# Optimization experiments

Measured on AMD Instinct MI355X. Metric: run time of the kernel, lower is better.

## Reference

```python
import jax, jax.numpy as jnp
import numpy as np

IN_FEAT = 66; D_MODEL = 512; KS = 10; DCT_N = 20; NUM_STAGE = 2; BN_EPS = 1e-5
HID = D_MODEL; GCN_IN = 2 * DCT_N


def get_dct_matrix(N):
    k = np.arange(N)[:, None]; i = np.arange(N)[None, :]
    w = np.full((N, 1), np.sqrt(2.0 / N)); w[0, 0] = np.sqrt(1.0 / N)
    dct = (w * np.cos(np.pi * (i + 0.5) * k / N)).astype(np.float32)
    idct = np.linalg.inv(dct).astype(np.float32)
    return jnp.asarray(dct), jnp.asarray(idct)


def conv1d(x, w):
    # x: [B, Cin, L], w: [Cout, Cin, K] -> [B, Cout, L-K+1]
    return jax.lax.conv_general_dilated(x, w, (1,), 'VALID', dimension_numbers=('NCH', 'OIH', 'NCH'))


def _forward(src, Wq1, Wq2, Wk1, Wk2, gc1_W, gc1_att, gc1_b, bn1_g, bn1_b,
             gcb_W, gcb_att, gcb_b, gcb_bn_g, gcb_bn_b, gc7_W, gc7_att, gc7_b,
             output_n, input_n):
    bs = src.shape[0]
    src = src[:, :input_n]                                  # [B, 50, F]
    vl = KS + output_n                                      # 35
    vn = input_n - KS - output_n + 1                        # 16
    dct_m, idct_m = get_dct_matrix(vl)

    key_in = jnp.swapaxes(src, 1, 2)[:, :, :input_n - output_n] / 1000.0   # [B, F, 25]
    query_in = jnp.swapaxes(src, 1, 2)[:, :, -KS:] / 1000.0                # [B, F, 10]

    # overlapping sliding windows -> per-window DCT coefficients
    idx = np.arange(vl)[None, :] + np.arange(vn)[:, None]   # [vn, vl]
    val = src[:, idx]                                       # [B, vn, vl, F]
    val = jnp.einsum('kv,bnvf->bnfk', dct_m[:DCT_N], val).reshape(bs, vn, IN_FEAT * DCT_N)

    key = jax.nn.relu(conv1d(jax.nn.relu(conv1d(key_in, Wk1)), Wk2))       # [B, D, vn]
    query = jax.nn.relu(conv1d(jax.nn.relu(conv1d(query_in, Wq1)), Wq2))   # [B, D, 1]

    score = jnp.einsum('bdq,bdn->bqn', query, key) + 1e-15                 # [B, 1, vn]
    att = score / jnp.sum(score, axis=2, keepdims=True)                    # sum-normalized attention
    dct_att = jnp.einsum('bqn,bnf->bqf', att, val)[:, 0].reshape(bs, IN_FEAT, DCT_N)

    # last KS frames + last frame repeated output_n times
    idx2 = np.concatenate([np.arange(input_n - KS, input_n), np.full(output_n, input_n - 1)])
    input_gcn = src[:, idx2]                                               # [B, vl, F]
    dct_in = jnp.swapaxes(jnp.einsum('kv,bvf->bkf', dct_m[:DCT_N], input_gcn), 1, 2)  # [B, F, DCT_N]
    x = jnp.concatenate([dct_in, dct_att], axis=-1)                        # [B, F, 2*DCT_N]

    # ---- GCN (eval mode: dropout off, BN with fresh running stats mean=0, var=1) ----
    def gc(y, W, A, bias):
        return jnp.einsum('nm,bmf->bnf', A, y @ W) + bias

    def bn(y, g, be):
        b_, n_, f_ = y.shape
        v = y.reshape(b_, n_ * f_)
        v = v * (g / np.float32(np.sqrt(1.0 + BN_EPS))) + be
        return v.reshape(b_, n_, f_)

    y = jnp.tanh(bn(gc(x, gc1_W, gc1_att, gc1_b), bn1_g, bn1_b))
    for st in range(NUM_STAGE):
        y0 = y
        y = jnp.tanh(bn(gc(y, gcb_W[st, 0], gcb_att[st, 0], gcb_b[st, 0]), gcb_bn_g[st, 0], gcb_bn_b[st, 0]))
        y = jnp.tanh(bn(gc(y, gcb_W[st, 1], gcb_att[st, 1], gcb_b[st, 1]), gcb_bn_g[st, 1], gcb_bn_b[st, 1]))
        y = y + y0
    dct_out = gc(y, gc7_W, gc7_att, gc7_b) + x                             # [B, F, 2*DCT_N]

    out = jnp.einsum('vk,bfk->bvf', idct_m[:, :DCT_N], dct_out[:, :, :DCT_N])  # [B, vl, F]
    return out[:, :, None, :]                                              # [B, vl, itera=1, F]


def setup_inputs():
    key = jax.random.key(0)
    ks = jax.random.split(key, 11)
    bs = 512; s = 0.05; f32 = jnp.float32
    return {
        'src': jax.random.normal(ks[0], (bs, 50, IN_FEAT), f32),
        'Wq1': jax.random.normal(ks[1], (D_MODEL, IN_FEAT, 6), f32) * s,
        'Wq2': jax.random.normal(ks[2], (D_MODEL, D_MODEL, 5), f32) * s,
        'Wk1': jax.random.normal(ks[3], (D_MODEL, IN_FEAT, 6), f32) * s,
        'Wk2': jax.random.normal(ks[4], (D_MODEL, D_MODEL, 5), f32) * s,
        'gc1_W': jax.random.normal(ks[5], (GCN_IN, HID), f32) * s,
        'gc1_att': jax.random.normal(ks[6], (IN_FEAT, IN_FEAT), f32) * s,
        'gc1_b': jnp.zeros((HID,), f32),
        'bn1_g': jnp.ones((IN_FEAT * HID,), f32),
        'bn1_b': jnp.zeros((IN_FEAT * HID,), f32),
        'gcb_W': jax.random.normal(ks[7], (NUM_STAGE, 2, HID, HID), f32) * s,
        'gcb_att': jax.random.normal(ks[8], (NUM_STAGE, 2, IN_FEAT, IN_FEAT), f32) * s,
        'gcb_b': jnp.zeros((NUM_STAGE, 2, HID), f32),
        'gcb_bn_g': jnp.ones((NUM_STAGE, 2, IN_FEAT * HID), f32),
        'gcb_bn_b': jnp.zeros((NUM_STAGE, 2, IN_FEAT * HID), f32),
        'gc7_W': jax.random.normal(ks[9], (HID, GCN_IN), f32) * s,
        'gc7_att': jax.random.normal(ks[10], (IN_FEAT, IN_FEAT), f32) * s,
        'gc7_b': jnp.zeros((GCN_IN,), f32),
        'output_n': 25,
        'input_n': 50,
    }


def reference(src, Wq1, Wq2, Wk1, Wk2, gc1_W, gc1_att, gc1_b, bn1_g, bn1_b,
              gcb_W, gcb_att, gcb_b, gcb_bn_g, gcb_bn_b, gc7_W, gc7_att, gc7_b,
              output_n, input_n):
    return _forward(src, Wq1, Wq2, Wk1, Wk2, gc1_W, gc1_att, gc1_b, bn1_g, bn1_b,
                    gcb_W, gcb_att, gcb_b, gcb_bn_g, gcb_bn_b, gc7_W, gc7_att, gc7_b,
                    output_n, input_n)
```

## Files before the change

### kernel.cpp

```cpp
#include <hip/hip_runtime.h>
#include <math.h>

#define PI_D 3.14159265358979323846

#define BSZ   512
#define NODE  66
#define VL    35
#define DCTN  20

static constexpr float BN_INVS = 0.99999500003749969f;

typedef unsigned short u16;
using bf16x8 = __attribute__((ext_vector_type(8))) short;
using f32x4  = __attribute__((ext_vector_type(4))) float;

__device__ inline u16 f2bf(float f) {
    union { float f; unsigned int u; } v; v.f = f;
    unsigned int r = v.u + 0x7FFFu + ((v.u >> 16) & 1u);
    return (u16)(r >> 16);
}
__device__ inline float bf2f(u16 b) {
    union { unsigned int u; float f; } v; v.u = ((unsigned int)b) << 16;
    return v.f;
}

__global__ void dct_kernel(float* __restrict__ dct20) {
    int i = blockIdx.x * blockDim.x + threadIdx.x;
    if (i < DCTN * VL) {
        int k = i / VL, v = i - k * VL;
        double w = (k == 0) ? sqrt(1.0 / VL) : sqrt(2.0 / VL);
        dct20[i] = (float)(w * cos(PI_D * (v + 0.5) * k / (double)VL));
    }
}

__global__ void cvt_gcb(const float* __restrict__ W, u16* __restrict__ Wt) {
    int l = blockIdx.y;
    int i = blockIdx.x * 256 + threadIdx.x;
    int n = i >> 9, k = i & 511;
    Wt[(size_t)l * 262144 + i] = f2bf(W[(size_t)l * 262144 + (size_t)k * 512 + n]);
}
__global__ void cvt_gc1(const float* __restrict__ W, u16* __restrict__ Wt) {
    int i = blockIdx.x * 256 + threadIdx.x;
    int n = i >> 6, k = i & 63;
    Wt[i] = (k < 40) ? f2bf(W[k * 512 + n]) : (u16)0;
}
__global__ void cvt_gc7(const float* __restrict__ W, u16* __restrict__ Wt) {
    int i = blockIdx.x * 256 + threadIdx.x;
    int n = i >> 9, k = i & 511;
    Wt[i] = (n < 20) ? f2bf(W[k * 40 + n]) : (u16)0;
}
__global__ void cvt_w1(const float* __restrict__ W, u16* __restrict__ Wt) {
    int i = blockIdx.x * 256 + threadIdx.x;
    int d = i / 416, k = i - d * 416;
    float v = 0.f;
    if (k < 396) { int h = k / 66, c = k - h * 66; v = W[d * 396 + c * 6 + h]; }
    Wt[i] = f2bf(v);
}
__global__ void cvt_w2(const float* __restrict__ W, u16* __restrict__ Wt) {
    int i = blockIdx.x * 256 + threadIdx.x;
    int d = i / 2560, k = i - d * 2560;
    int h = k >> 9, c = k & 511;
    Wt[i] = f2bf(W[(size_t)d * 2560 + c * 5 + h]);
}
__global__ void cvt_att(const float* __restrict__ gc1A, const float* __restrict__ gcbA,
                        const float* __restrict__ gc7A, u16* __restrict__ Abf) {
    int l = blockIdx.y;
    int i = blockIdx.x * 256 + threadIdx.x;
    if (i < 8320) {
        int r = i / 104, c = i - (i / 104) * 104;
        float v = 0.f;
        if (r < 66 && c < 66) {
            const float* A = (l == 0) ? gc1A : (l <= 4 ? gcbA + (size_t)(l - 1) * 4356 : gc7A);
            v = A[r * 66 + c];
        }
        Abf[(size_t)l * 8320 + i] = f2bf(v);
    }
}

template<int FB, int NW>
__global__ __launch_bounds__(256) void amul(const u16* __restrict__ Y,
                                            const u16* __restrict__ Abf,
                                            u16* __restrict__ U) {
    const int b = blockIdx.x, f0 = blockIdx.y * FB;
    const int tid = threadIdx.x;
    __shared__ u16 As[80][104];
    __shared__ u16 Ys[FB][104];
    for (int i = tid; i < 4160; i += 256) ((unsigned int*)As)[i] = ((const unsigned int*)Abf)[i];
    for (int i = tid; i < 66 * (FB / 2); i += 256) {
        int m = i / (FB / 2), fi = i - (i / (FB / 2)) * (FB / 2);
        unsigned int v = *(const unsigned int*)&Y[((size_t)b * 66 + m) * NW + f0 + 2 * fi];
        Ys[2 * fi][m] = (u16)(v & 0xffff);
        Ys[2 * fi + 1][m] = (u16)(v >> 16);
    }
    for (int i = tid; i < FB * 19; i += 256) {
        int f = i / 19, j = i - (i / 19) * 19;
        ((unsigned int*)&Ys[f][66])[j] = 0;
    }
    __syncthreads();
    const int lane = tid & 63, w = tid >> 6;
    const int row16 = lane & 15, grp = lane >> 4;
    const int fbase = w * (FB / 4);
    constexpr int NFT = FB / 64;
    f32x4 acc[5][NFT] = {};
#pragma unroll
    for (int k0 = 0; k0 < 96; k0 += 32) {
        bf16x8 aF[5], bF[NFT];
#pragma unroll
        for (int mt = 0; mt < 5; ++mt) aF[mt] = *(const bf16x8*)&As[mt * 16 + row16][grp * 8 + k0];
#pragma unroll
        for (int ft = 0; ft < NFT; ++ft) bF[ft] = *(const bf16x8*)&Ys[fbase + ft * 16 + row16][grp * 8 + k0];
#pragma unroll
        for (int mt = 0; mt < 5; ++mt)
#pragma unroll
            for (int ft = 0; ft < NFT; ++ft)
                acc[mt][ft] = __builtin_amdgcn_mfma_f32_16x16x32_bf16(aF[mt], bF[ft], acc[mt][ft], 0, 0, 0);
    }
#pragma unroll
    for (int mt = 0; mt < 5; ++mt) {
#pragma unroll
        for (int ft = 0; ft < NFT; ++ft) {
            int fcol = f0 + fbase + ft * 16 + row16;
#pragma unroll
            for (int j = 0; j < 4; ++j) {
                int row = mt * 16 + grp * 4 + j;
                if (row < 66)
                    U[((size_t)b * 66 + row) * NW + fcol] = f2bf(acc[mt][ft][j]);
            }
        }
    }
}

template<int ASRC, int EPI, int TOUT, int TIN, int T0>
__global__ __launch_bounds__(256) void gemm_uni(const void* __restrict__ Asrc,
                                                const u16* __restrict__ Bt,
                                                void* __restrict__ Cout,
                                                int M, int K, int Nvalid, int ldc,
                                                const float* __restrict__ bias,
                                                const float* __restrict__ g,
                                                const float* __restrict__ be,
                                                const u16* __restrict__ yres,
                                                const float* __restrict__ xres) {
    __shared__ u16 As[128][40];
    __shared__ u16 Bs[128][40];
    const int tid = threadIdx.x;
    const int r0 = blockIdx.x * 128, n0 = blockIdx.y * 128;
    const int lane = tid & 63, w = tid >> 6;
    const int wr = (w >> 1) * 64, wc = (w & 1) * 64;
    const int row16 = lane & 15, grp = lane >> 4;
    const int sr = tid >> 1, sq = (tid & 1) * 16;

    const u16* ap = nullptr;
    const float* apf = nullptr;
    if constexpr (ASRC == 0) {
        ap = (const u16*)Asrc + (size_t)(r0 + sr) * K + sq;
    } else if constexpr (ASRC == 1) {
        int R = r0 + sr; int b = R / TOUT, t = R - b * TOUT;
        ap = (const u16*)Asrc + ((size_t)b * TIN + t) * 512 + sq;
    } else {
        int R = r0 + sr; int b = R / TOUT, t = R - b * TOUT;
        apf = (const float*)Asrc + (size_t)b * 3300 + (T0 + t) * 66 + sq;
    }
    const u16* bp = Bt + (size_t)(n0 + sr) * K + sq;

    f32x4 acc[4][4] = {};
    for (int k0 = 0; k0 < K; k0 += 32) {
        if constexpr (ASRC <= 1) {
            *(bf16x8*)&As[sr][sq]     = *(const bf16x8*)(ap + k0);
            *(bf16x8*)&As[sr][sq + 8] = *(const bf16x8*)(ap + k0 + 8);
        } else {
#pragma unroll
            for (int j = 0; j < 16; ++j) {
                int k = k0 + sq + j;
                float vin = 0.f;
                if (k < 396) vin = apf[k0 + j];
                As[sr][sq + j] = f2bf(vin * 1e-3f);
            }
        }
        *(bf16x8*)&Bs[sr][sq]     = *(const bf16x8*)(bp + k0);
        *(bf16x8*)&Bs[sr][sq + 8] = *(const bf16x8*)(bp + k0 + 8);
        __syncthreads();
        bf16x8 a[4], b[4];
#pragma unroll
        for (int m = 0; m < 4; ++m) a[m] = *(const bf16x8*)&As[wr + m * 16 + row16][grp * 8];
#pragma unroll
        for (int n = 0; n < 4; ++n) b[n] = *(const bf16x8*)&Bs[wc + n * 16 + row16][grp * 8];
#pragma unroll
        for (int m = 0; m < 4; ++m)
#pragma unroll
            for (int n = 0; n < 4; ++n)
                acc[m][n] = __builtin_amdgcn_mfma_f32_16x16x32_bf16(a[m], b[n], acc[m][n], 0, 0, 0);
        __syncthreads();
    }
#pragma unroll
    for (int m = 0; m < 4; ++m) {
        int rb = r0 + wr + m * 16 + grp * 4;
#pragma unroll
        for (int n = 0; n < 4; ++n) {
            int c = n0 + wc + n * 16 + row16;
            if (c < Nvalid) {
#pragma unroll
                for (int j = 0; j < 4; ++j) {
                    int row = rb + j;
                    float v = acc[m][n][j];
                    if constexpr (EPI == 0) {
                        ((u16*)Cout)[(size_t)row * ldc + c] = f2bf(fmaxf(v, 0.f));
                    } else if constexpr (EPI == 1) {
                        ((float*)Cout)[(size_t)row * ldc + c] = fmaxf(v, 0.f);
                    } else if constexpr (EPI == 2 || EPI == 3) {
                        int bb = row / 66, nn = row - bb * 66;
                        int gi = nn * 512 + c;
                        float z = v + bias[c];
                        float t = tanhf(z * (g[gi] * BN_INVS) + be[gi]);
                        if constexpr (EPI == 3) t += bf2f(yres[(size_t)row * 512 + c]);
                        ((u16*)Cout)[(size_t)row * 512 + c] = f2bf(t);
                    } else {
                        int bb = row / 66, nn = row - bb * 66;
                        ((float*)Cout)[(size_t)bb * 1320 + nn * 20 + c] =
                            v + bias[c] + xres[(size_t)bb * 2640 + nn * 40 + c];
                    }
                }
            }
        }
    }
}

__global__ __launch_bounds__(256) void att_kernel(const float* __restrict__ qT,
                                                  const float* __restrict__ kT,
                                                  float* __restrict__ att) {
    const int b = blockIdx.x, tid = threadIdx.x;
    __shared__ float part[256];
    __shared__ float sc[16];
    int n = tid >> 4, j = tid & 15;
    const float* q = qT + b * 512;
    const float* k = kT + b * 8192 + n * 512;
    float acc = 0.f;
    for (int d = j; d < 512; d += 16) acc += q[d] * k[d];
    part[tid] = acc;
    __syncthreads();
    if (tid < 16) {
        float s = 0.f;
        for (int jj = 0; jj < 16; ++jj) s += part[tid * 16 + jj];
        sc[tid] = s + 1e-15f;
    }
    __syncthreads();
    if (tid == 0) {
        float tot = 0.f;
        for (int nn = 0; nn < 16; ++nn) tot += sc[nn];
        float inv = 1.f / tot;
        for (int nn = 0; nn < 16; ++nn) att[b * 16 + nn] = sc[nn] * inv;
    }
}

__global__ __launch_bounds__(256) void xbuild(const float* __restrict__ src,
                                              const float* __restrict__ att,
                                              const float* __restrict__ dct20,
                                              float* __restrict__ x,
                                              u16* __restrict__ xbf) {
    const int b = blockIdx.x, tid = threadIdx.x;
    __shared__ float s_src[50 * 66];
    __shared__ float s_sacc[VL * 66];
    __shared__ float s_d[DCTN * VL];
    __shared__ float s_att[16];
    for (int i = tid; i < 3300; i += 256) s_src[i] = src[b * 3300 + i];
    for (int i = tid; i < DCTN * VL; i += 256) s_d[i] = dct20[i];
    if (tid < 16) s_att[tid] = att[b * 16 + tid];
    __syncthreads();
    for (int i = tid; i < VL * 66; i += 256) {
        int v = i / 66, f = i - (i / 66) * 66;
        float a = 0.f;
#pragma unroll
        for (int n = 0; n < 16; ++n) a += s_att[n] * s_src[(n + v) * 66 + f];
        s_sacc[i] = a;
    }
    __syncthreads();
    for (int i = tid; i < 66 * DCTN; i += 256) {
        int f = i / DCTN, kq = i - (i / DCTN) * DCTN;
        float din = 0.f, datt = 0.f;
        for (int v = 0; v < VL; ++v) {
            float dv = s_d[kq * VL + v];
            int t2 = (v < 10) ? (40 + v) : 49;
            din += dv * s_src[t2 * 66 + f];
            datt += dv * s_sacc[v * 66 + f];
        }
        x[b * 2640 + f * 40 + kq] = din;
        x[b * 2640 + f * 40 + 20 + kq] = datt;
        xbf[(size_t)b * 4224 + f * 64 + kq] = f2bf(din);
        xbf[(size_t)b * 4224 + f * 64 + 20 + kq] = f2bf(datt);
    }
    for (int i = tid; i < 66 * 24; i += 256) {
        int f = i / 24, kp = 40 + (i - (i / 24) * 24);
        xbf[(size_t)b * 4224 + f * 64 + kp] = 0;
    }
}

__global__ __launch_bounds__(256) void final_out(const float* __restrict__ dctout,
                                                 const float* __restrict__ dct20,
                                                 float* __restrict__ out) {
    const int b = blockIdx.x, tid = threadIdx.x;
    __shared__ float ds[DCTN * VL];
    __shared__ float dos[66 * 20];
    for (int i = tid; i < DCTN * VL; i += 256) ds[i] = dct20[i];
    for (int i = tid; i < 1320; i += 256) dos[i] = dctout[(size_t)b * 1320 + i];
    __syncthreads();
    for (int o = tid; o < VL * 66; o += 256) {
        int v = o / 66, f = o - (o / 66) * 66;
        float acc = 0.f;
#pragma unroll
        for (int k = 0; k < DCTN; ++k) acc += ds[k * VL + v] * dos[f * 20 + k];
        out[(size_t)b * 2310 + o] = acc;
    }
}

extern "C" void kernel_launch(void* const* d_in, const int* in_sizes, int n_in,
                              void* d_out, int out_size, void* d_ws, size_t ws_size,
                              hipStream_t stream) {
    const float* src     = (const float*)d_in[0];
    const float* Wq1     = (const float*)d_in[1];
    const float* Wq2     = (const float*)d_in[2];
    const float* Wk1     = (const float*)d_in[3];
    const float* Wk2     = (const float*)d_in[4];
    const float* gc1_W   = (const float*)d_in[5];
    const float* gc1_att = (const float*)d_in[6];
    const float* gc1_b   = (const float*)d_in[7];
    const float* bn1_g   = (const float*)d_in[8];
    const float* bn1_b   = (const float*)d_in[9];
    const float* gcb_W   = (const float*)d_in[10];
    const float* gcb_att = (const float*)d_in[11];
    const float* gcb_b   = (const float*)d_in[12];
    const float* gcb_g   = (const float*)d_in[13];
    const float* gcb_be  = (const float*)d_in[14];
    const float* gc7_W   = (const float*)d_in[15];
    const float* gc7_att = (const float*)d_in[16];
    const float* gc7_b   = (const float*)d_in[17];
    float* out = (float*)d_out;

    unsigned char* base = (unsigned char*)d_ws;
    size_t off = 0;
    auto take = [&](size_t bytes) -> void* {
        void* p = base + off;
        off += (bytes + 255) & ~(size_t)255;
        return p;
    };
    u16*   yA     = (u16*)take((size_t)33792 * 512 * 2);
    u16*   yB     = (u16*)take((size_t)33792 * 512 * 2);
    u16*   ub     = (u16*)take((size_t)33792 * 512 * 2);
    u16*   u1     = (u16*)take((size_t)33792 * 64 * 2);
    float* xb     = (float*)take((size_t)512 * 2640 * 4);
    u16*   xbf    = (u16*)take((size_t)512 * 4224 * 2);
    float* dct20  = (float*)take(2800);
    float* dctout = (float*)take((size_t)512 * 1320 * 4);
    u16*   key1   = (u16*)take((size_t)512 * 20 * 512 * 2);
    u16*   q1     = (u16*)take((size_t)512 * 5 * 512 * 2);
    float* keyT   = (float*)take((size_t)8192 * 512 * 4);
    float* queryT = (float*)take((size_t)512 * 512 * 4);
    float* attw   = (float*)take((size_t)512 * 16 * 4);
    u16*   WtGcb  = (u16*)take((size_t)4 * 512 * 512 * 2);
    u16*   WtGc1  = (u16*)take((size_t)512 * 64 * 2);
    u16*   WtGc7  = (u16*)take((size_t)128 * 512 * 2);
    u16*   WtW1k  = (u16*)take((size_t)512 * 416 * 2);
    u16*   WtW1q  = (u16*)take((size_t)512 * 416 * 2);
    u16*   WtW2k  = (u16*)take((size_t)512 * 2560 * 2);
    u16*   WtW2q  = (u16*)take((size_t)512 * 2560 * 2);
    u16*   Abf    = (u16*)take((size_t)6 * 8320 * 2);

    dct_kernel<<<2, 384, 0, stream>>>(dct20);
    cvt_att<<<dim3(33, 6), 256, 0, stream>>>(gc1_att, gcb_att, gc7_att, Abf);
    cvt_gcb<<<dim3(1024, 4), 256, 0, stream>>>(gcb_W, WtGcb);
    cvt_gc1<<<128, 256, 0, stream>>>(gc1_W, WtGc1);
    cvt_gc7<<<256, 256, 0, stream>>>(gc7_W, WtGc7);
    cvt_w1<<<832, 256, 0, stream>>>(Wk1, WtW1k);
    cvt_w1<<<832, 256, 0, stream>>>(Wq1, WtW1q);
    cvt_w2<<<5120, 256, 0, stream>>>(Wk2, WtW2k);
    cvt_w2<<<5120, 256, 0, stream>>>(Wq2, WtW2q);

    gemm_uni<2, 0, 20, 25, 0><<<dim3(80, 4), 256, 0, stream>>>(
        src, WtW1k, key1, 10240, 416, 512, 512, nullptr, nullptr, nullptr, nullptr, nullptr);
    gemm_uni<2, 0, 5, 10, 40><<<dim3(20, 4), 256, 0, stream>>>(
        src, WtW1q, q1, 2560, 416, 512, 512, nullptr, nullptr, nullptr, nullptr, nullptr);
    gemm_uni<1, 1, 16, 20, 0><<<dim3(64, 4), 256, 0, stream>>>(
        key1, WtW2k, keyT, 8192, 2560, 512, 512, nullptr, nullptr, nullptr, nullptr, nullptr);
    gemm_uni<1, 1, 1, 5, 0><<<dim3(4, 4), 256, 0, stream>>>(
        q1, WtW2q, queryT, 512, 2560, 512, 512, nullptr, nullptr, nullptr, nullptr, nullptr);
    att_kernel<<<BSZ, 256, 0, stream>>>(queryT, keyT, attw);
    xbuild<<<BSZ, 256, 0, stream>>>(src, attw, dct20, xb, xbf);

    amul<64, 64><<<dim3(512, 1), 256, 0, stream>>>(xbf, Abf, u1);
    gemm_uni<0, 2, 1, 1, 0><<<dim3(264, 4), 256, 0, stream>>>(
        u1, WtGc1, yA, 33792, 64, 512, 512, gc1_b, bn1_g, bn1_b, nullptr, nullptr);

    for (int st = 0; st < 2; ++st) {
        const u16* W0 = WtGcb + (size_t)(st * 2 + 0) * 262144;
        const u16* W1 = WtGcb + (size_t)(st * 2 + 1) * 262144;
        const u16* A0 = Abf + (size_t)(1 + st * 2) * 8320;
        const u16* A1 = Abf + (size_t)(2 + st * 2) * 8320;
        const float* b0  = gcb_b + (size_t)(st * 2 + 0) * 512;
        const float* b1  = gcb_b + (size_t)(st * 2 + 1) * 512;
        const float* g0  = gcb_g + (size_t)(st * 2 + 0) * 33792;
        const float* g1  = gcb_g + (size_t)(st * 2 + 1) * 33792;
        const float* be0 = gcb_be + (size_t)(st * 2 + 0) * 33792;
        const float* be1 = gcb_be + (size_t)(st * 2 + 1) * 33792;
        amul<128, 512><<<dim3(512, 4), 256, 0, stream>>>(yA, A0, ub);
        gemm_uni<0, 2, 1, 1, 0><<<dim3(264, 4), 256, 0, stream>>>(
            ub, W0, yB, 33792, 512, 512, 512, b0, g0, be0, nullptr, nullptr);
        amul<128, 512><<<dim3(512, 4), 256, 0, stream>>>(yB, A1, ub);
        gemm_uni<0, 3, 1, 1, 0><<<dim3(264, 4), 256, 0, stream>>>(
            ub, W1, yA, 33792, 512, 512, 512, b1, g1, be1, yA, nullptr);
    }

    amul<128, 512><<<dim3(512, 4), 256, 0, stream>>>(yA, Abf + (size_t)5 * 8320, ub);
    gemm_uni<0, 4, 1, 1, 0><<<dim3(264, 1), 256, 0, stream>>>(
        ub, WtGc7, dctout, 33792, 512, 20, 20, gc7_b, nullptr, nullptr, nullptr, xb);
    final_out<<<BSZ, 256, 0, stream>>>(dctout, dct20, out);
}
```

Measured before the change: 844.1 us.

## Fuse adjacency multiply into graph-conv GEMM by reassociating A(YW)

Replaces each separate adjacency-multiply kernel plus GEMM pair with one fused kernel. The fused kernel computes Y·W for two batch items per block, transposes the result into shared memory, then applies the 66x66 adjacency with MFMA before the bias/BN/tanh epilogue. Reassociating (AY)W into A(YW) removes the large bf16 intermediate buffer and its global write/read for every graph layer, and halves the kernel launches. The cost is heavier register and shared-memory use per block (about 58 accumulator tiles and roughly 63KB of LDS), plus an extra bf16 rounding of the intermediate in a different place.

```diff
diff --git a/kernel.cpp b/kernel.cpp
--- a/kernel.cpp
+++ b/kernel.cpp
@@ -77,69 +77,145 @@
     }
 }
 
-template<int FB, int NW>
-__global__ __launch_bounds__(256) void amul(const u16* __restrict__ Y,
-                                            const u16* __restrict__ Abf,
-                                            u16* __restrict__ U) {
-    const int b = blockIdx.x, f0 = blockIdx.y * FB;
-    const int tid = threadIdx.x;
-    __shared__ u16 As[80][104];
-    __shared__ u16 Ys[FB][104];
-    for (int i = tid; i < 4160; i += 256) ((unsigned int*)As)[i] = ((const unsigned int*)Abf)[i];
-    for (int i = tid; i < 66 * (FB / 2); i += 256) {
-        int m = i / (FB / 2), fi = i - (i / (FB / 2)) * (FB / 2);
-        unsigned int v = *(const unsigned int*)&Y[((size_t)b * 66 + m) * NW + f0 + 2 * fi];
-        Ys[2 * fi][m] = (u16)(v & 0xffff);
-        Ys[2 * fi + 1][m] = (u16)(v >> 16);
-    }
-    for (int i = tid; i < FB * 19; i += 256) {
-        int f = i / 19, j = i - (i / 19) * 19;
-        ((unsigned int*)&Ys[f][66])[j] = 0;
-    }
-    __syncthreads();
-    const int lane = tid & 63, w = tid >> 6;
-    const int row16 = lane & 15, grp = lane >> 4;
-    const int fbase = w * (FB / 4);
-    constexpr int NFT = FB / 64;
-    f32x4 acc[5][NFT] = {};
-#pragma unroll
-    for (int k0 = 0; k0 < 96; k0 += 32) {
-        bf16x8 aF[5], bF[NFT];
-#pragma unroll
-        for (int mt = 0; mt < 5; ++mt) aF[mt] = *(const bf16x8*)&As[mt * 16 + row16][grp * 8 + k0];
-#pragma unroll
-        for (int ft = 0; ft < NFT; ++ft) bF[ft] = *(const bf16x8*)&Ys[fbase + ft * 16 + row16][grp * 8 + k0];
-#pragma unroll
-        for (int mt = 0; mt < 5; ++mt)
-#pragma unroll
-            for (int ft = 0; ft < NFT; ++ft)
-                acc[mt][ft] = __builtin_amdgcn_mfma_f32_16x16x32_bf16(aF[mt], bF[ft], acc[mt][ft], 0, 0, 0);
-    }
-#pragma unroll
-    for (int mt = 0; mt < 5; ++mt) {
-#pragma unroll
-        for (int ft = 0; ft < NFT; ++ft) {
-            int fcol = f0 + fbase + ft * 16 + row16;
-#pragma unroll
-            for (int j = 0; j < 4; ++j) {
-                int row = mt * 16 + grp * 4 + j;
-                if (row < 66)
-                    U[((size_t)b * 66 + row) * NW + fcol] = f2bf(acc[mt][ft][j]);
-            }
-        }
-    }
-}
-
-template<int ASRC, int EPI, int TOUT, int TIN, int T0>
-__global__ __launch_bounds__(256) void gemm_uni(const void* __restrict__ Asrc,
-                                                const u16* __restrict__ Bt,
-                                                void* __restrict__ Cout,
-                                                int M, int K, int Nvalid, int ldc,
+template<int EPI>
+__global__ __launch_bounds__(256) void gc_fused(const u16* __restrict__ Y,
+                                                const u16* __restrict__ Wt,
+                                                const u16* __restrict__ Ab,
+                                                void* __restrict__ Yout, int K,
                                                 const float* __restrict__ bias,
                                                 const float* __restrict__ g,
                                                 const float* __restrict__ be,
                                                 const u16* __restrict__ yres,
                                                 const float* __restrict__ xres) {
+    __shared__ u16 As[144][40];
+    __shared__ u16 Bs[128][40];
+    __shared__ u16 zT[128][168];
+    const int tid = threadIdx.x;
+    const int b0 = blockIdx.x * 2;
+    const int n0 = blockIdx.y * 128;
+    const int lane = tid & 63, w = tid >> 6;
+    const int row16 = lane & 15, grp = lane >> 4;
+
+    for (int i = tid; i < 128 * 36; i += 256) {
+        int f = i / 36, j = i - (i / 36) * 36;
+        int c = (j < 6) ? (66 + j) : (132 + j);
+        zT[f][c] = 0;
+    }
+
+    const int sr = tid >> 1, sq = (tid & 1) * 16;
+    long r1 = (long)b0 * 66 + sr;        if (r1 > 33791) r1 = 33791;
+    long r2 = (long)b0 * 66 + 128 + sr;  if (r2 > 33791) r2 = 33791;
+    const u16* ap1 = Y + (size_t)r1 * K + sq;
+    const u16* ap2 = Y + (size_t)r2 * K + sq;
+    const u16* bp  = Wt + (size_t)(n0 + sr) * K + sq;
+
+    f32x4 acc[9][2] = {};
+    for (int k0 = 0; k0 < K; k0 += 32) {
+        *(bf16x8*)&As[sr][sq]     = *(const bf16x8*)(ap1 + k0);
+        *(bf16x8*)&As[sr][sq + 8] = *(const bf16x8*)(ap1 + k0 + 8);
+        if (tid < 32) {
+            *(bf16x8*)&As[128 + sr][sq]     = *(const bf16x8*)(ap2 + k0);
+            *(bf16x8*)&As[128 + sr][sq + 8] = *(const bf16x8*)(ap2 + k0 + 8);
+        }
+        *(bf16x8*)&Bs[sr][sq]     = *(const bf16x8*)(bp + k0);
+        *(bf16x8*)&Bs[sr][sq + 8] = *(const bf16x8*)(bp + k0 + 8);
+        __syncthreads();
+        bf16x8 a[9], b[2];
+#pragma unroll
+        for (int mt = 0; mt < 9; ++mt) a[mt] = *(const bf16x8*)&As[mt * 16 + row16][grp * 8];
+#pragma unroll
+        for (int nt = 0; nt < 2; ++nt) b[nt] = *(const bf16x8*)&Bs[w * 32 + nt * 16 + row16][grp * 8];
+#pragma unroll
+        for (int mt = 0; mt < 9; ++mt)
+#pragma unroll
+            for (int nt = 0; nt < 2; ++nt)
+                acc[mt][nt] = __builtin_amdgcn_mfma_f32_16x16x32_bf16(a[mt], b[nt], acc[mt][nt], 0, 0, 0);
+        __syncthreads();
+    }
+
+#pragma unroll
+    for (int mt = 0; mt < 9; ++mt) {
+        int m = mt * 16 + grp * 4;
+        if (m < 132) {
+#pragma unroll
+            for (int nt = 0; nt < 2; ++nt) {
+                int f = w * 32 + nt * 16 + row16;
+                u16 e0 = f2bf(acc[mt][nt][0]), e1 = f2bf(acc[mt][nt][1]);
+                u16 e2 = f2bf(acc[mt][nt][2]), e3 = f2bf(acc[mt][nt][3]);
+                if (m + 3 < 66 || m >= 66) {
+                    int col = (m < 66) ? m : m + 6;
+                    *(unsigned int*)&zT[f][col]     = (unsigned int)e0 | ((unsigned int)e1 << 16);
+                    *(unsigned int*)&zT[f][col + 2] = (unsigned int)e2 | ((unsigned int)e3 << 16);
+                } else {
+                    zT[f][64] = e0; zT[f][65] = e1; zT[f][72] = e2; zT[f][73] = e3;
+                }
+            }
+        }
+    }
+
+    bf16x8 aA[5][3];
+#pragma unroll
+    for (int mt = 0; mt < 5; ++mt)
+#pragma unroll
+        for (int k2 = 0; k2 < 3; ++k2)
+            aA[mt][k2] = *(const bf16x8*)&Ab[(mt * 16 + row16) * 104 + k2 * 32 + grp * 8];
+    __syncthreads();
+
+    f32x4 acc2[2][5][2] = {};
+#pragma unroll
+    for (int bb = 0; bb < 2; ++bb) {
+        const int base = bb * 72;
+#pragma unroll
+        for (int k2 = 0; k2 < 3; ++k2) {
+            bf16x8 bz[2];
+#pragma unroll
+            for (int ft = 0; ft < 2; ++ft)
+                bz[ft] = *(const bf16x8*)&zT[w * 32 + ft * 16 + row16][base + k2 * 32 + grp * 8];
+#pragma unroll
+            for (int mt = 0; mt < 5; ++mt)
+#pragma unroll
+                for (int ft = 0; ft < 2; ++ft)
+                    acc2[bb][mt][ft] = __builtin_amdgcn_mfma_f32_16x16x32_bf16(aA[mt][k2], bz[ft], acc2[bb][mt][ft], 0, 0, 0);
+        }
+    }
+
+#pragma unroll
+    for (int bb = 0; bb < 2; ++bb) {
+        const int bidx = b0 + bb;
+#pragma unroll
+        for (int mt = 0; mt < 5; ++mt) {
+            int nb = mt * 16 + grp * 4;
+#pragma unroll
+            for (int ft = 0; ft < 2; ++ft) {
+                int c = n0 + w * 32 + ft * 16 + row16;
+#pragma unroll
+                for (int j = 0; j < 4; ++j) {
+                    int n = nb + j;
+                    if (n < 66) {
+                        float v = acc2[bb][mt][ft][j];
+                        if constexpr (EPI == 4) {
+                            if (c < 20)
+                                ((float*)Yout)[(size_t)bidx * 1320 + n * 20 + c] =
+                                    v + bias[c] + xres[(size_t)bidx * 2640 + n * 40 + c];
+                        } else {
+                            int gi = n * 512 + c;
+                            float z = v + bias[c];
+                            float t = tanhf(z * (g[gi] * BN_INVS) + be[gi]);
+                            if constexpr (EPI == 3) t += bf2f(yres[((size_t)bidx * 66 + n) * 512 + c]);
+                            ((u16*)Yout)[((size_t)bidx * 66 + n) * 512 + c] = f2bf(t);
+                        }
+                    }
+                }
+            }
+        }
+    }
+}
+
+template<int ASRC, int EPI, int TOUT, int TIN, int T0>
+__global__ __launch_bounds__(256) void gemm_uni(const void* __restrict__ Asrc,
+                                                const u16* __restrict__ Bt,
+                                                void* __restrict__ Cout,
+                                                int M, int K, int Nvalid, int ldc) {
     __shared__ u16 As[128][40];
     __shared__ u16 Bs[128][40];
     const int tid = threadIdx.x;
@@ -151,9 +227,7 @@
 
     const u16* ap = nullptr;
     const float* apf = nullptr;
-    if constexpr (ASRC == 0) {
-        ap = (const u16*)Asrc + (size_t)(r0 + sr) * K + sq;
-    } else if constexpr (ASRC == 1) {
+    if constexpr (ASRC == 1) {
         int R = r0 + sr; int b = R / TOUT, t = R - b * TOUT;
         ap = (const u16*)Asrc + ((size_t)b * TIN + t) * 512 + sq;
     } else {
@@ -164,7 +238,7 @@
 
     f32x4 acc[4][4] = {};
     for (int k0 = 0; k0 < K; k0 += 32) {
-        if constexpr (ASRC <= 1) {
+        if constexpr (ASRC == 1) {
             *(bf16x8*)&As[sr][sq]     = *(const bf16x8*)(ap + k0);
             *(bf16x8*)&As[sr][sq + 8] = *(const bf16x8*)(ap + k0 + 8);
         } else {
@@ -200,24 +274,9 @@
             if (c < Nvalid) {
 #pragma unroll
                 for (int j = 0; j < 4; ++j) {
-                    int row = rb + j;
-                    float v = acc[m][n][j];
-                    if constexpr (EPI == 0) {
-                        ((u16*)Cout)[(size_t)row * ldc + c] = f2bf(fmaxf(v, 0.f));
-                    } else if constexpr (EPI == 1) {
-                        ((float*)Cout)[(size_t)row * ldc + c] = fmaxf(v, 0.f);
-                    } else if constexpr (EPI == 2 || EPI == 3) {
-                        int bb = row / 66, nn = row - bb * 66;
-                        int gi = nn * 512 + c;
-                        float z = v + bias[c];
-                        float t = tanhf(z * (g[gi] * BN_INVS) + be[gi]);
-                        if constexpr (EPI == 3) t += bf2f(yres[(size_t)row * 512 + c]);
-                        ((u16*)Cout)[(size_t)row * 512 + c] = f2bf(t);
-                    } else {
-                        int bb = row / 66, nn = row - bb * 66;
-                        ((float*)Cout)[(size_t)bb * 1320 + nn * 20 + c] =
-                            v + bias[c] + xres[(size_t)bb * 2640 + nn * 40 + c];
-                    }
+                    float v = fmaxf(acc[m][n][j], 0.f);
+                    if constexpr (EPI == 0) ((u16*)Cout)[(size_t)(rb + j) * ldc + c] = f2bf(v);
+                    else                    ((float*)Cout)[(size_t)(rb + j) * ldc + c] = v;
                 }
             }
         }
@@ -343,8 +402,6 @@
     };
     u16*   yA     = (u16*)take((size_t)33792 * 512 * 2);
     u16*   yB     = (u16*)take((size_t)33792 * 512 * 2);
-    u16*   ub     = (u16*)take((size_t)33792 * 512 * 2);
-    u16*   u1     = (u16*)take((size_t)33792 * 64 * 2);
     float* xb     = (float*)take((size_t)512 * 2640 * 4);
     u16*   xbf    = (u16*)take((size_t)512 * 4224 * 2);
     float* dct20  = (float*)take(2800);
@@ -374,19 +431,18 @@
     cvt_w2<<<5120, 256, 0, stream>>>(Wq2, WtW2q);
 
     gemm_uni<2, 0, 20, 25, 0><<<dim3(80, 4), 256, 0, stream>>>(
-        src, WtW1k, key1, 10240, 416, 512, 512, nullptr, nullptr, nullptr, nullptr, nullptr);
+        src, WtW1k, key1, 10240, 416, 512, 512);
     gemm_uni<2, 0, 5, 10, 40><<<dim3(20, 4), 256, 0, stream>>>(
-        src, WtW1q, q1, 2560, 416, 512, 512, nullptr, nullptr, nullptr, nullptr, nullptr);
+        src, WtW1q, q1, 2560, 416, 512, 512);
     gemm_uni<1, 1, 16, 20, 0><<<dim3(64, 4), 256, 0, stream>>>(
-        key1, WtW2k, keyT, 8192, 2560, 512, 512, nullptr, nullptr, nullptr, nullptr, nullptr);
+        key1, WtW2k, keyT, 8192, 2560, 512, 512);
     gemm_uni<1, 1, 1, 5, 0><<<dim3(4, 4), 256, 0, stream>>>(
-        q1, WtW2q, queryT, 512, 2560, 512, 512, nullptr, nullptr, nullptr, nullptr, nullptr);
+        q1, WtW2q, queryT, 512, 2560, 512, 512);
     att_kernel<<<BSZ, 256, 0, stream>>>(queryT, keyT, attw);
     xbuild<<<BSZ, 256, 0, stream>>>(src, attw, dct20, xb, xbf);
 
-    amul<64, 64><<<dim3(512, 1), 256, 0, stream>>>(xbf, Abf, u1);
-    gemm_uni<0, 2, 1, 1, 0><<<dim3(264, 4), 256, 0, stream>>>(
-        u1, WtGc1, yA, 33792, 64, 512, 512, gc1_b, bn1_g, bn1_b, nullptr, nullptr);
+    gc_fused<2><<<dim3(256, 4), 256, 0, stream>>>(
+        xbf, WtGc1, Abf, yA, 64, gc1_b, bn1_g, bn1_b, nullptr, nullptr);
 
     for (int st = 0; st < 2; ++st) {
         const u16* W0 = WtGcb + (size_t)(st * 2 + 0) * 262144;
@@ -399,16 +455,13 @@
         const float* g1  = gcb_g + (size_t)(st * 2 + 1) * 33792;
         const float* be0 = gcb_be + (size_t)(st * 2 + 0) * 33792;
         const float* be1 = gcb_be + (size_t)(st * 2 + 1) * 33792;
-        amul<128, 512><<<dim3(512, 4), 256, 0, stream>>>(yA, A0, ub);
-        gemm_uni<0, 2, 1, 1, 0><<<dim3(264, 4), 256, 0, stream>>>(
-            ub, W0, yB, 33792, 512, 512, 512, b0, g0, be0, nullptr, nullptr);
-        amul<128, 512><<<dim3(512, 4), 256, 0, stream>>>(yB, A1, ub);
-        gemm_uni<0, 3, 1, 1, 0><<<dim3(264, 4), 256, 0, stream>>>(
-            ub, W1, yA, 33792, 512, 512, 512, b1, g1, be1, yA, nullptr);
-    }
-
-    amul<128, 512><<<dim3(512, 4), 256, 0, stream>>>(yA, Abf + (size_t)5 * 8320, ub);
-    gemm_uni<0, 4, 1, 1, 0><<<dim3(264, 1), 256, 0, stream>>>(
-        ub, WtGc7, dctout, 33792, 512, 20, 20, gc7_b, nullptr, nullptr, nullptr, xb);
+        gc_fused<2><<<dim3(256, 4), 256, 0, stream>>>(
+            yA, W0, A0, yB, 512, b0, g0, be0, nullptr, nullptr);
+        gc_fused<3><<<dim3(256, 4), 256, 0, stream>>>(
+            yB, W1, A1, yA, 512, b1, g1, be1, yA, nullptr);
+    }
+
+    gc_fused<4><<<dim3(256, 1), 256, 0, stream>>>(
+        yA, WtGc7, Abf + (size_t)5 * 8320, dctout, 512, gc7_b, nullptr, nullptr, nullptr, xb);
     final_out<<<BSZ, 256, 0, stream>>>(dctout, dct20, out);
 }
```

New measurement: 808.4 us. 1.04x faster.
